# Kernel optimization log

Hardware: AMD Instinct MI355X
Metric: run time of the kernel (lower is better)

## Reference

```python
import jax, jax.numpy as jnp
import numpy as np

N_VISITS, N_PROC, N_MED = 64, 32, 16
V_DIAG, V_PROC, V_MED = 2000, 1500, 4000
EMB, EMB_FF = 256, 128


def _normalize(adj):
    # row-normalize(adj + I), matching GCN.normalize
    adj = adj + np.eye(adj.shape[0], dtype=np.float32)
    rs = adj.sum(1)
    rinv = np.where(rs > 0, 1.0 / rs, 0.0).astype(np.float32)
    return (adj * rinv[:, None]).astype(np.float32)


def setup_inputs() -> dict:
    key = jax.random.key(0)
    ks = jax.random.split(key, 24)
    rng = np.random.default_rng(0)
    ehr = (rng.random((V_MED, V_MED)) < 0.01).astype(np.float32)
    ddi = (rng.random((V_MED, V_MED)) < 0.01).astype(np.float32)
    s = 0.02
    return {
        'proc_codes': jax.random.randint(ks[0], (N_VISITS, N_PROC), 0, V_DIAG + V_PROC + 2),
        'med_codes': jax.random.randint(ks[1], (N_VISITS, N_MED), 0, V_MED),
        'emb_table': jax.random.normal(ks[2], (V_DIAG + V_PROC + 2, EMB_FF)) * s,
        'conv_w': jax.random.normal(ks[3], (3,)) * 0.3,
        'conv_b': jnp.zeros((1,)),
        'wq': jax.random.normal(ks[4], (EMB_FF, EMB)) * s,
        'wk': jax.random.normal(ks[5], (EMB_FF, EMB)) * s,
        'wv': jax.random.normal(ks[6], (EMB_FF, EMB)) * s,
        'wr': jax.random.normal(ks[7], (EMB, EMB)) * s,
        'alpha': jax.random.normal(ks[8], (EMB,)),
        'beta': jax.random.normal(ks[9], (EMB,)),
        'ehr_adj_norm': jnp.asarray(_normalize(ehr)),
        'ddi_adj_norm': jnp.asarray(_normalize(ddi)),
        'ddi_adj_raw': jnp.asarray(ddi),
        'ehr_w1': jax.random.normal(ks[10], (V_MED, EMB)) * s,
        'ehr_b1': jnp.zeros((EMB,)),
        'ehr_w2': jax.random.normal(ks[11], (EMB, EMB)) * s,
        'ehr_b2': jnp.zeros((EMB,)),
        'ddi_w1': jax.random.normal(ks[12], (V_MED, EMB)) * s,
        'ddi_b1': jnp.zeros((EMB,)),
        'ddi_w2': jax.random.normal(ks[13], (EMB, EMB)) * s,
        'ddi_b2': jnp.zeros((EMB,)),
        'inter': jax.random.normal(ks[14], (1,)) * 0.1,
        'out_w1': jax.random.normal(ks[15], (3 * EMB, 2 * EMB)) * s,
        'out_b1': jnp.zeros((2 * EMB,)),
        'out_w2': jax.random.normal(ks[16], (2 * EMB, V_MED)) * s,
        'out_b2': jnp.zeros((V_MED,)),
    }


def _fastformer(x, wq, wk, wv, wr, alpha, beta):
    # x: (1, n, EMB_FF); additive linear attention (all-ones mask => no-op)
    q = x @ wq  # (1, n, EMB)
    k = x @ wk
    v = x @ wv
    scale = EMB ** -0.5
    aw = jax.nn.softmax(q * alpha * scale, axis=-1)
    gq = jnp.sum(q * aw, axis=1)              # global query (1, EMB)
    p = gq[:, None, :] * k                    # (1, n, EMB)
    bw = jax.nn.softmax(p * beta * scale, axis=-1)
    gk = jnp.sum(p * bw, axis=1)              # global key (1, EMB)
    return (gk[:, None, :] * v) @ wr + q


def _gcn(adj, w1, b1, w2, b2):
    # input x = I, so first layer support is just w1
    h = jax.nn.relu(adj @ w1 + b1)
    return adj @ (h @ w2) + b2


def reference(proc_codes, med_codes, emb_table, conv_w, conv_b, wq, wk, wv, wr, alpha, beta,
              ehr_adj_norm, ddi_adj_norm, ddi_adj_raw,
              ehr_w1, ehr_b1, ehr_w2, ehr_b2, ddi_w1, ddi_b1, ddi_w2, ddi_b2,
              inter, out_w1, out_b1, out_w2, out_b2):
    n = proc_codes.shape[0]
    # per-admission mean embedding  (n, EMB_FF)
    i2 = emb_table[proc_codes].mean(axis=1)
    # Conv1d(1,1,k=3,same) over the feature dim, then ReLU
    xp = jnp.pad(i2, ((0, 0), (1, 1)))
    i2 = jax.nn.relu(conv_w[0] * xp[:, :-2] + conv_w[1] * xp[:, 1:-1] + conv_w[2] * xp[:, 2:] + conv_b)
    feat = _fastformer(i2[None], wq, wk, wv, wr, alpha, beta)[0]  # (n, EMB)
    query = feat[-1:]
    drug_memory = _gcn(ehr_adj_norm, ehr_w1, ehr_b1, ehr_w2, ehr_b2) \
        - _gcn(ddi_adj_norm, ddi_w1, ddi_b1, ddi_w2, ddi_b2) * inter[0]
    key_w1 = jax.nn.softmax(query @ drug_memory.T, axis=-1)   # (1, V_MED)
    fact1 = key_w1 @ drug_memory                              # (1, EMB)
    # history (len(input) > 1): multi-hot med history values
    history_keys = feat[:-1]
    hv = jnp.zeros((n - 1, V_MED), dtype=feat.dtype)
    hv = hv.at[jnp.arange(n - 1)[:, None], med_codes[:-1]].set(1.0)
    visit_w = jax.nn.softmax(query @ history_keys.T, axis=-1)
    fact2 = (visit_w @ hv) @ drug_memory
    h = jnp.concatenate([query, fact1, fact2], axis=-1)       # (1, 3*EMB)
    result = jax.nn.relu(h @ out_w1 + out_b1) @ out_w2 + out_b2
    sp = jax.nn.sigmoid(result)[0]
    batch_neg = 0.0005 * jnp.einsum('i,ij,j->', sp, ddi_adj_raw, sp)
    return result, batch_neg
```

## Files before the change

kernel.cpp:

```cpp
#include <hip/hip_runtime.h>
#include <hip/hip_bf16.h>

#define NV 64
#define NP 32
#define NM 16
#define VMED 4000
#define EMB 256
#define EMBFF 128
#define CAP 128
#define GR 4


__device__ __forceinline__ float block_sum_256(float v, float* red) {
    int t = threadIdx.x;
    red[t] = v; __syncthreads();
    for (int s = 128; s > 0; s >>= 1) { if (t < s) red[t] += red[t + s]; __syncthreads(); }
    float r = red[0]; __syncthreads();
    return r;
}
__device__ __forceinline__ float block_max_256(float v, float* red) {
    int t = threadIdx.x;
    red[t] = v; __syncthreads();
    for (int s = 128; s > 0; s >>= 1) { if (t < s) red[t] = fmaxf(red[t], red[t + s]); __syncthreads(); }
    float r = red[0]; __syncthreads();
    return r;
}

__global__ void k_ff1(const int* __restrict__ proc, const float* __restrict__ emb,
                      const float* __restrict__ cw, const float* __restrict__ cb,
                      const float* __restrict__ wq, const float* __restrict__ wk,
                      const float* __restrict__ wv, const float* __restrict__ alpha,
                      float* __restrict__ q, float* __restrict__ k, float* __restrict__ v,
                      float* __restrict__ qaw) {
    __shared__ float sm[EMBFF + 2];
    __shared__ float x[EMBFF];
    __shared__ float red[256];
    int vi = blockIdx.x, t = threadIdx.x;
    if (t < EMBFF) {
        float s = 0.f;
        for (int c = 0; c < NP; c++) s += emb[proc[vi * NP + c] * EMBFF + t];
        sm[t + 1] = s * (1.0f / NP);
    }
    if (t == 0) { sm[0] = 0.f; sm[EMBFF + 1] = 0.f; }
    __syncthreads();
    if (t < EMBFF) {
        float o = cw[0] * sm[t] + cw[1] * sm[t + 1] + cw[2] * sm[t + 2] + cb[0];
        x[t] = o > 0.f ? o : 0.f;
    }
    __syncthreads();
    float aq = 0, ak = 0, av = 0;
    for (int e = 0; e < EMBFF; e++) {
        float xe = x[e];
        aq += xe * wq[e * EMB + t];
        ak += xe * wk[e * EMB + t];
        av += xe * wv[e * EMB + t];
    }
    q[vi * EMB + t] = aq; k[vi * EMB + t] = ak; v[vi * EMB + t] = av;
    const float scale = 0.0625f;
    float z = aq * alpha[t] * scale;
    float m = block_max_256(z, red);
    float e_ = __expf(z - m);
    float sum = block_sum_256(e_, red);
    qaw[vi * EMB + t] = aq * (e_ / sum);
}

__global__ void k_pbw(const float* __restrict__ qaw, const float* __restrict__ k,
                      const float* __restrict__ beta, float* __restrict__ pbw) {
    __shared__ float red[256];
    int vi = blockIdx.x, f = threadIdx.x;
    float g = 0;
    for (int r = 0; r < NV; r++) g += qaw[r * EMB + f];
    float p = g * k[vi * EMB + f];
    const float scale = 0.0625f;
    float z = p * beta[f] * scale;
    float m = block_max_256(z, red);
    float e_ = __expf(z - m);
    float sum = block_sum_256(e_, red);
    pbw[vi * EMB + f] = p * (e_ / sum);
}

__global__ void k_feat(const float* __restrict__ pbw, const float* __restrict__ v,
                       const float* __restrict__ q, const float* __restrict__ wr,
                       float* __restrict__ feat) {
    __shared__ float s[EMB];
    int vi = blockIdx.x, f = threadIdx.x;
    float g = 0;
    for (int r = 0; r < NV; r++) g += pbw[r * EMB + f];
    s[f] = g * v[vi * EMB + f];
    __syncthreads();
    float acc = 0;
    for (int e = 0; e < EMB; e++) acc += s[e] * wr[e * EMB + f];
    feat[vi * EMB + f] = acc + q[vi * EMB + f];
}

__global__ void k_visitw_wmed(const float* __restrict__ feat, const int* __restrict__ med,
                              float* __restrict__ w_med) {
    __shared__ float qs[EMB];
    __shared__ float vw[64];
    __shared__ float red[256];
    __shared__ float wm[VMED];
    int t = threadIdx.x;
    for (int e = t; e < EMB; e += 256) qs[e] = feat[63 * EMB + e];
    for (int i = t; i < VMED; i += 256) wm[i] = 0.f;
    __syncthreads();
    float sc = -1e30f;
    if (t < 63) {
        float a = 0;
        for (int e = 0; e < EMB; e++) a += qs[e] * feat[t * EMB + e];
        sc = a;
    }
    float m = block_max_256(sc, red);
    float e_ = (t < 63) ? __expf(sc - m) : 0.f;
    float sum = block_sum_256(e_, red);
    if (t < 63) vw[t] = e_ / sum;
    __syncthreads();
    for (int i = t; i < 63 * NM; i += 256) {
        int vv = i / NM, mm = i % NM;
        int code = med[vv * NM + mm];
        bool dup = false;
        for (int m2 = 0; m2 < mm; m2++)
            if (med[vv * NM + m2] == code) dup = true;
        if (!dup) atomicAdd(&wm[code], vw[vv]);
    }
    __syncthreads();
    for (int i = t; i < VMED; i += 256) w_med[i] = wm[i];
}

__global__ void k_gcn(const float* __restrict__ eadj, const float* __restrict__ dadj,
                      const float* __restrict__ ew1, const float* __restrict__ eb1,
                      const float* __restrict__ ew2,
                      const float* __restrict__ dw1, const float* __restrict__ db1,
                      const float* __restrict__ dw2,
                      float* __restrict__ outE, float* __restrict__ outD,
                      int* __restrict__ ccntE, int* __restrict__ cidxE, float* __restrict__ cvalE,
                      int* __restrict__ ccntD, int* __restrict__ cidxD, float* __restrict__ cvalD) {
    __shared__ float x[GR][EMB];
    __shared__ int idx[GR][CAP];
    __shared__ float val[GR][CAP];
    __shared__ int cnt[GR];
    int b = blockIdx.x, t = threadIdx.x;
    bool isD = b >= 1000;
    const float* adj = isD ? dadj : eadj;
    const float* w1  = isD ? dw1  : ew1;
    const float* b1  = isD ? db1  : eb1;
    const float* w2  = isD ? dw2  : ew2;
    float* outp = isD ? outD : outE;
    int*   ccnt = isD ? ccntD : ccntE;
    int*   cidx = isD ? cidxD : cidxE;
    float* cval = isD ? cvalD : cvalE;
    int r0 = (isD ? b - 1000 : b) * GR;
    if (t < GR) cnt[t] = 0;
    __syncthreads();

    const float4* base4 = (const float4*)(adj + (size_t)r0 * VMED);
    const int Q = VMED / 4;
    for (int jj = t; jj < GR * Q; jj += 256) {
        float4 a = base4[jj];
        int r = jj / Q;
        int c0 = (jj - r * Q) * 4;
        if (a.x != 0.f) { int p = atomicAdd(&cnt[r], 1); if (p < CAP) { idx[r][p] = c0;     val[r][p] = a.x; } }
        if (a.y != 0.f) { int p = atomicAdd(&cnt[r], 1); if (p < CAP) { idx[r][p] = c0 + 1; val[r][p] = a.y; } }
        if (a.z != 0.f) { int p = atomicAdd(&cnt[r], 1); if (p < CAP) { idx[r][p] = c0 + 2; val[r][p] = a.z; } }
        if (a.w != 0.f) { int p = atomicAdd(&cnt[r], 1); if (p < CAP) { idx[r][p] = c0 + 3; val[r][p] = a.w; } }
    }
    __syncthreads();

    for (int r = 0; r < GR; r++) {
        int n = cnt[r] < CAP ? cnt[r] : CAP;
        if (t == 0) ccnt[r0 + r] = n;
        if (t < n) { cidx[(r0 + r) * CAP + t] = idx[r][t]; cval[(r0 + r) * CAP + t] = val[r][t]; }
        float acc = b1[t];
        for (int e = 0; e < n; e++) acc += val[r][e] * w1[(size_t)idx[r][e] * EMB + t];
        x[r][t] = acc > 0.f ? acc : 0.f;
    }
    __syncthreads();

    float a[GR];
    #pragma unroll
    for (int r = 0; r < GR; r++) a[r] = 0.f;
    #pragma unroll 4
    for (int e = 0; e < EMB; e++) {
        float we = w2[e * EMB + t];
        #pragma unroll
        for (int r = 0; r < GR; r++) a[r] += x[r][e] * we;
    }
    for (int r = 0; r < GR; r++) outp[(size_t)(r0 + r) * EMB + t] = a[r];
}

__global__ void k_acc(const int* __restrict__ ccntE, const int* __restrict__ cidxE,
                      const float* __restrict__ cvalE,
                      const int* __restrict__ ccntD, const int* __restrict__ cidxD,
                      const float* __restrict__ cvalD,
                      const float* __restrict__ xe, const float* __restrict__ xd,
                      const float* __restrict__ b2e, const float* __restrict__ b2d,
                      const float* __restrict__ inter, const float* __restrict__ feat,
                      float* __restrict__ dm, float* __restrict__ sdm) {
    __shared__ int idxE[CAP];
    __shared__ float valE[CAP];
    __shared__ int idxD[CAP];
    __shared__ float valD[CAP];
    __shared__ float red[256];
    int i = blockIdx.x, t = threadIdx.x;
    int nE = ccntE[i], nD = ccntD[i];
    if (t < nE) { idxE[t] = cidxE[i * CAP + t]; valE[t] = cvalE[i * CAP + t]; }
    if (t < nD) { idxD[t] = cidxD[i * CAP + t]; valD[t] = cvalD[i * CAP + t]; }
    __syncthreads();
    float aE = b2e[t];
    for (int e = 0; e < nE; e++) aE += valE[e] * xe[(size_t)idxE[e] * EMB + t];
    float aD = b2d[t];
    for (int e = 0; e < nD; e++) aD += valD[e] * xd[(size_t)idxD[e] * EMB + t];
    float dmv = aE - inter[0] * aD;
    dm[(size_t)i * EMB + t] = dmv;
    float s = block_sum_256(dmv * feat[63 * EMB + t], red);
    if (t == 0) sdm[i] = s;
}

__global__ void k_softmax4000(const float* __restrict__ s, float* __restrict__ out) {
    __shared__ float red[256];
    int t = threadIdx.x;
    float m = -1e30f;
    for (int i = t; i < VMED; i += 256) m = fmaxf(m, s[i]);
    m = block_max_256(m, red);
    float sum = 0;
    for (int i = t; i < VMED; i += 256) { float e = __expf(s[i] - m); out[i] = e; sum += e; }
    sum = block_sum_256(sum, red);
    float inv = 1.f / sum;
    for (int i = t; i < VMED; i += 256) out[i] *= inv;
}

__global__ void k_facts_part(const float* __restrict__ dm, const float* __restrict__ kw,
                             const float* __restrict__ wm, float* __restrict__ part1,
                             float* __restrict__ part2) {
    int f = threadIdx.x, b = blockIdx.x;
    int r0 = b * 100;
    float a1 = 0, a2 = 0;
    for (int r = r0; r < r0 + 100; r++) {
        float d = dm[(size_t)r * EMB + f];
        a1 += kw[r] * d;
        a2 += wm[r] * d;
    }
    part1[b * EMB + f] = a1;
    part2[b * EMB + f] = a2;
}

__global__ void k_hidden_part(const float* __restrict__ feat, const float* __restrict__ part1,
                              const float* __restrict__ part2, const float* __restrict__ w1,
                              float* __restrict__ hpart) {
    __shared__ float xs[16];
    int b = blockIdx.x, t = threadIdx.x;
    int e0 = b * 16;
    if (t < 16) {
        int e = e0 + t;
        float xv;
        if (e < 256) xv = feat[63 * EMB + e];
        else if (e < 512) { float s = 0; for (int p = 0; p < 40; p++) s += part1[p * EMB + (e - 256)]; xv = s; }
        else              { float s = 0; for (int p = 0; p < 40; p++) s += part2[p * EMB + (e - 512)]; xv = s; }
        xs[t] = xv;
    }
    __syncthreads();
    float a1 = 0, a2 = 0;
    #pragma unroll
    for (int i = 0; i < 16; i++) {
        int e = e0 + i;
        a1 += xs[i] * w1[e * 512 + t];
        a2 += xs[i] * w1[e * 512 + t + 256];
    }
    hpart[b * 512 + t] = a1;
    hpart[b * 512 + t + 256] = a2;
}

__global__ void k_result(const float* __restrict__ hpart, const float* __restrict__ b1,
                         const float* __restrict__ w2, const float* __restrict__ b2,
                         float* __restrict__ out, float* __restrict__ sp) {
    __shared__ float hx[512];
    __shared__ float red[8][32];
    int t = threadIdx.x;
    for (int jj = t; jj < 512; jj += 256) {
        float s = b1[jj];
        for (int p = 0; p < 48; p++) s += hpart[p * 512 + jj];
        hx[jj] = s > 0.f ? s : 0.f;
    }
    __syncthreads();
    int lane = t & 31, seg = t >> 5;
    int j = blockIdx.x * 32 + lane;
    float acc = 0;
    int e0 = seg * 64;
    #pragma unroll 8
    for (int e = e0; e < e0 + 64; e++) acc += hx[e] * w2[(size_t)e * VMED + j];
    red[seg][lane] = acc;
    __syncthreads();
    if (seg == 0) {
        float s = b2[j];
        for (int p = 0; p < 8; p++) s += red[p][lane];
        out[j] = s;
        sp[j] = 1.f / (1.f + __expf(-s));
    }
}

__global__ void k_bneg(const float* __restrict__ ddi, const float* __restrict__ sp,
                       float* __restrict__ bpart) {
    __shared__ float4 spl[VMED / 4];
    __shared__ float red[8][256];
    int t = threadIdx.x;
    const float4* sp4 = (const float4*)sp;
    for (int j4 = t; j4 < VMED / 4; j4 += 256) spl[j4] = sp4[j4];
    __syncthreads();
    int i0 = blockIdx.x * 8;
    const float4* row4 = (const float4*)(ddi + (size_t)i0 * VMED);
    float p[8] = {0, 0, 0, 0, 0, 0, 0, 0};
    for (int j4 = t; j4 < VMED / 4; j4 += 256) {
        float4 s4 = spl[j4];
        #pragma unroll
        for (int rr = 0; rr < 8; rr++) {
            float4 a = row4[rr * (VMED / 4) + j4];
            p[rr] += a.x * s4.x + a.y * s4.y + a.z * s4.z + a.w * s4.w;
        }
    }
    #pragma unroll
    for (int rr = 0; rr < 8; rr++) red[rr][t] = p[rr];
    __syncthreads();
    for (int s = 128; s > 0; s >>= 1) {
        if (t < s) {
            #pragma unroll
            for (int rr = 0; rr < 8; rr++) red[rr][t] += red[rr][t + s];
        }
        __syncthreads();
    }
    if (t < 8) bpart[i0 + t] = sp[i0 + t] * red[t][0];
}

__global__ void FastRx_wo_Diag_19473381720179_kernel(const float* __restrict__ bpart,
                                                     float* __restrict__ out) {
    __shared__ float red[256];
    int t = threadIdx.x;
    float s = 0;
    for (int i = t; i < VMED; i += 256) s += bpart[i];
    s = block_sum_256(s, red);
    if (t == 0) out[VMED] = 0.0005f * s;
}

extern "C" __attribute__((visibility("default")))
void kernel_launch(void* const* d_in, const int* in_sizes, int n_in,
                   void* d_out, int out_size, void* d_ws, size_t ws_size,
                   hipStream_t stream) {
    const int*   proc_codes = (const int*)d_in[0];
    const int*   med_codes  = (const int*)d_in[1];
    const float* emb_table  = (const float*)d_in[2];
    const float* conv_w     = (const float*)d_in[3];
    const float* conv_b     = (const float*)d_in[4];
    const float* wq         = (const float*)d_in[5];
    const float* wk         = (const float*)d_in[6];
    const float* wv         = (const float*)d_in[7];
    const float* wr         = (const float*)d_in[8];
    const float* alpha      = (const float*)d_in[9];
    const float* beta       = (const float*)d_in[10];
    const float* ehr_adj    = (const float*)d_in[11];
    const float* ddi_adj    = (const float*)d_in[12];
    const float* ddi_raw    = (const float*)d_in[13];
    const float* ehr_w1     = (const float*)d_in[14];
    const float* ehr_b1     = (const float*)d_in[15];
    const float* ehr_w2     = (const float*)d_in[16];
    const float* ehr_b2     = (const float*)d_in[17];
    const float* ddi_w1     = (const float*)d_in[18];
    const float* ddi_b1     = (const float*)d_in[19];
    const float* ddi_w2     = (const float*)d_in[20];
    const float* ddi_b2     = (const float*)d_in[21];
    const float* inter      = (const float*)d_in[22];
    const float* out_w1     = (const float*)d_in[23];
    const float* out_b1     = (const float*)d_in[24];
    const float* out_w2     = (const float*)d_in[25];
    const float* out_b2     = (const float*)d_in[26];
    float* out = (float*)d_out;

    float* w = (float*)d_ws;
    float* q      = w;
    float* k      = w + 16384;
    float* v      = w + 32768;
    float* tmpA   = w + 49152;
    float* tmpB   = w + 65536;
    float* feat   = w + 81920;
    float* wmed   = w + 98304;
    float* sdm    = w + 102400;
    float* sp     = w + 106496;
    float* bufA   = w + 110592;
    float* bufC   = bufA + 1024000;
    float* bufB   = bufC + 1024000;
    int*   ccntE  = (int*)(bufB + 1024000);
    int*   cidxE  = ccntE + 4096;
    float* cvalE  = (float*)(cidxE + 512000);
    int*   ccntD  = (int*)(cvalE + 512000);
    int*   cidxD  = ccntD + 4096;
    float* cvalD  = (float*)(cidxD + 512000);
    float* part1  = bufA;
    float* part2  = bufA + 10240;
    float* hpart  = bufA + 20480;
    float* bpart  = bufA + 45056;

    k_ff1<<<NV, EMB, 0, stream>>>(proc_codes, emb_table, conv_w, conv_b,
                                  wq, wk, wv, alpha, q, k, v, tmpA);
    k_pbw<<<NV, EMB, 0, stream>>>(tmpA, k, beta, tmpB);
    k_feat<<<NV, EMB, 0, stream>>>(tmpB, v, q, wr, feat);
    k_visitw_wmed<<<1, 256, 0, stream>>>(feat, med_codes, wmed);

    k_gcn<<<2000, 256, 0, stream>>>(ehr_adj, ddi_adj,
                                    ehr_w1, ehr_b1, ehr_w2,
                                    ddi_w1, ddi_b1, ddi_w2,
                                    bufA, bufC,
                                    ccntE, cidxE, cvalE, ccntD, cidxD, cvalD);
    k_acc<<<VMED, 256, 0, stream>>>(ccntE, cidxE, cvalE, ccntD, cidxD, cvalD,
                                    bufA, bufC, ehr_b2, ddi_b2, inter, feat,
                                    bufB, sdm);

    k_softmax4000<<<1, 256, 0, stream>>>(sdm, sdm);
    k_facts_part<<<40, 256, 0, stream>>>(bufB, sdm, wmed, part1, part2);
    k_hidden_part<<<48, 256, 0, stream>>>(feat, part1, part2, out_w1, hpart);
    k_result<<<125, 256, 0, stream>>>(hpart, out_b1, out_w2, out_b2, out, sp);
    k_bneg<<<VMED / 8, 256, 0, stream>>>(ddi_raw, sp, bpart);
    FastRx_wo_Diag_19473381720179_kernel<<<1, 256, 0, stream>>>(bpart, out);
}
```

Before: 409.1 us.

## Split GCN into per-row sparse scan kernel and batched gather-matmul kernel

After: 412.9 us. About the same (+0.9%).

```diff
diff --git a/kernel.cpp b/kernel.cpp
--- a/kernel.cpp
+++ b/kernel.cpp
@@ -8,7 +8,6 @@
 #define EMB 256
 #define EMBFF 128
 #define CAP 128
-#define GR 4
 
 
 __device__ __forceinline__ float block_sum_256(float v, float* red) {
@@ -126,65 +125,95 @@
     for (int i = t; i < VMED; i += 256) w_med[i] = wm[i];
 }
 
-__global__ void k_gcn(const float* __restrict__ eadj, const float* __restrict__ dadj,
-                      const float* __restrict__ ew1, const float* __restrict__ eb1,
-                      const float* __restrict__ ew2,
-                      const float* __restrict__ dw1, const float* __restrict__ db1,
-                      const float* __restrict__ dw2,
-                      float* __restrict__ outE, float* __restrict__ outD,
-                      int* __restrict__ ccntE, int* __restrict__ cidxE, float* __restrict__ cvalE,
-                      int* __restrict__ ccntD, int* __restrict__ cidxD, float* __restrict__ cvalD) {
-    __shared__ float x[GR][EMB];
-    __shared__ int idx[GR][CAP];
-    __shared__ float val[GR][CAP];
-    __shared__ int cnt[GR];
+__global__ void k_scan(const float* __restrict__ eadj, const float* __restrict__ dadj,
+                       int* __restrict__ ccntE, int* __restrict__ cidxE, float* __restrict__ cvalE,
+                       int* __restrict__ ccntD, int* __restrict__ cidxD, float* __restrict__ cvalD) {
+    __shared__ int idx[CAP];
+    __shared__ float val[CAP];
+    __shared__ int cnt;
     int b = blockIdx.x, t = threadIdx.x;
-    bool isD = b >= 1000;
+    bool isD = b >= VMED;
+    int i = isD ? b - VMED : b;
     const float* adj = isD ? dadj : eadj;
-    const float* w1  = isD ? dw1  : ew1;
-    const float* b1  = isD ? db1  : eb1;
-    const float* w2  = isD ? dw2  : ew2;
-    float* outp = isD ? outD : outE;
     int*   ccnt = isD ? ccntD : ccntE;
     int*   cidx = isD ? cidxD : cidxE;
     float* cval = isD ? cvalD : cvalE;
-    int r0 = (isD ? b - 1000 : b) * GR;
-    if (t < GR) cnt[t] = 0;
-    __syncthreads();
-
-    const float4* base4 = (const float4*)(adj + (size_t)r0 * VMED);
-    const int Q = VMED / 4;
-    for (int jj = t; jj < GR * Q; jj += 256) {
-        float4 a = base4[jj];
-        int r = jj / Q;
-        int c0 = (jj - r * Q) * 4;
-        if (a.x != 0.f) { int p = atomicAdd(&cnt[r], 1); if (p < CAP) { idx[r][p] = c0;     val[r][p] = a.x; } }
-        if (a.y != 0.f) { int p = atomicAdd(&cnt[r], 1); if (p < CAP) { idx[r][p] = c0 + 1; val[r][p] = a.y; } }
-        if (a.z != 0.f) { int p = atomicAdd(&cnt[r], 1); if (p < CAP) { idx[r][p] = c0 + 2; val[r][p] = a.z; } }
-        if (a.w != 0.f) { int p = atomicAdd(&cnt[r], 1); if (p < CAP) { idx[r][p] = c0 + 3; val[r][p] = a.w; } }
-    }
-    __syncthreads();
-
-    for (int r = 0; r < GR; r++) {
-        int n = cnt[r] < CAP ? cnt[r] : CAP;
-        if (t == 0) ccnt[r0 + r] = n;
-        if (t < n) { cidx[(r0 + r) * CAP + t] = idx[r][t]; cval[(r0 + r) * CAP + t] = val[r][t]; }
+    if (t == 0) cnt = 0;
+    __syncthreads();
+    const float4* row4 = (const float4*)(adj + (size_t)i * VMED);
+    for (int j4 = t; j4 < VMED / 4; j4 += 256) {
+        float4 a = row4[j4];
+        int c0 = j4 * 4;
+        if (a.x != 0.f) { int p = atomicAdd(&cnt, 1); if (p < CAP) { idx[p] = c0;     val[p] = a.x; } }
+        if (a.y != 0.f) { int p = atomicAdd(&cnt, 1); if (p < CAP) { idx[p] = c0 + 1; val[p] = a.y; } }
+        if (a.z != 0.f) { int p = atomicAdd(&cnt, 1); if (p < CAP) { idx[p] = c0 + 2; val[p] = a.z; } }
+        if (a.w != 0.f) { int p = atomicAdd(&cnt, 1); if (p < CAP) { idx[p] = c0 + 3; val[p] = a.w; } }
+    }
+    __syncthreads();
+    int n = cnt < CAP ? cnt : CAP;
+    if (t == 0) ccnt[i] = n;
+    if (t < n) { cidx[i * CAP + t] = idx[t]; cval[i * CAP + t] = val[t]; }
+}
+
+__global__ void k_gcn2(const int* __restrict__ ccntE, const int* __restrict__ cidxE,
+                       const float* __restrict__ cvalE,
+                       const int* __restrict__ ccntD, const int* __restrict__ cidxD,
+                       const float* __restrict__ cvalD,
+                       const float* __restrict__ ew1, const float* __restrict__ eb1,
+                       const float* __restrict__ ew2,
+                       const float* __restrict__ dw1, const float* __restrict__ db1,
+                       const float* __restrict__ dw2,
+                       float* __restrict__ outE, float* __restrict__ outD) {
+    __shared__ float x[8][EMB];
+    __shared__ int idx[8][CAP];
+    __shared__ float val[8][CAP];
+    __shared__ int nn8[8];
+    int b = blockIdx.x, t = threadIdx.x;
+    bool isD = b >= 500;
+    const int*   ccnt = isD ? ccntD : ccntE;
+    const int*   cidx = isD ? cidxD : cidxE;
+    const float* cval = isD ? cvalD : cvalE;
+    const float* w1   = isD ? dw1 : ew1;
+    const float* b1   = isD ? db1 : eb1;
+    const float* w2   = isD ? dw2 : ew2;
+    float* outp = isD ? outD : outE;
+    int r0 = (isD ? b - 500 : b) * 8;
+    for (int r = 0; r < 8; r++) {
+        int n = ccnt[r0 + r];
+        int n8 = (n + 7) & ~7;
+        if (t == 0) nn8[r] = n8;
+        if (t < n) { idx[r][t] = cidx[(r0 + r) * CAP + t]; val[r][t] = cval[(r0 + r) * CAP + t]; }
+        else if (t < n8) { idx[r][t] = 0; val[r][t] = 0.f; }
+    }
+    __syncthreads();
+    for (int r = 0; r < 8; r++) {
         float acc = b1[t];
-        for (int e = 0; e < n; e++) acc += val[r][e] * w1[(size_t)idx[r][e] * EMB + t];
+        int n8 = nn8[r];
+        for (int e = 0; e < n8; e += 8) {
+            float g0 = w1[(size_t)idx[r][e]     * EMB + t];
+            float g1 = w1[(size_t)idx[r][e + 1] * EMB + t];
+            float g2 = w1[(size_t)idx[r][e + 2] * EMB + t];
+            float g3 = w1[(size_t)idx[r][e + 3] * EMB + t];
+            float g4 = w1[(size_t)idx[r][e + 4] * EMB + t];
+            float g5 = w1[(size_t)idx[r][e + 5] * EMB + t];
+            float g6 = w1[(size_t)idx[r][e + 6] * EMB + t];
+            float g7 = w1[(size_t)idx[r][e + 7] * EMB + t];
+            acc += val[r][e]     * g0 + val[r][e + 1] * g1
+                 + val[r][e + 2] * g2 + val[r][e + 3] * g3
+                 + val[r][e + 4] * g4 + val[r][e + 5] * g5
+                 + val[r][e + 6] * g6 + val[r][e + 7] * g7;
+        }
         x[r][t] = acc > 0.f ? acc : 0.f;
     }
     __syncthreads();
-
-    float a[GR];
-    #pragma unroll
-    for (int r = 0; r < GR; r++) a[r] = 0.f;
+    float a[8] = {0, 0, 0, 0, 0, 0, 0, 0};
     #pragma unroll 4
     for (int e = 0; e < EMB; e++) {
         float we = w2[e * EMB + t];
         #pragma unroll
-        for (int r = 0; r < GR; r++) a[r] += x[r][e] * we;
-    }
-    for (int r = 0; r < GR; r++) outp[(size_t)(r0 + r) * EMB + t] = a[r];
+        for (int r = 0; r < 8; r++) a[r] += x[r][e] * we;
+    }
+    for (int r = 0; r < 8; r++) outp[(size_t)(r0 + r) * EMB + t] = a[r];
 }
 
 __global__ void k_acc(const int* __restrict__ ccntE, const int* __restrict__ cidxE,
@@ -202,13 +231,38 @@
     __shared__ float red[256];
     int i = blockIdx.x, t = threadIdx.x;
     int nE = ccntE[i], nD = ccntD[i];
+    int nE8 = (nE + 7) & ~7, nD8 = (nD + 7) & ~7;
     if (t < nE) { idxE[t] = cidxE[i * CAP + t]; valE[t] = cvalE[i * CAP + t]; }
+    else if (t < nE8) { idxE[t] = 0; valE[t] = 0.f; }
     if (t < nD) { idxD[t] = cidxD[i * CAP + t]; valD[t] = cvalD[i * CAP + t]; }
+    else if (t < nD8) { idxD[t] = 0; valD[t] = 0.f; }
     __syncthreads();
     float aE = b2e[t];
-    for (int e = 0; e < nE; e++) aE += valE[e] * xe[(size_t)idxE[e] * EMB + t];
+    for (int e = 0; e < nE8; e += 8) {
+        float g0 = xe[(size_t)idxE[e]     * EMB + t];
+        float g1 = xe[(size_t)idxE[e + 1] * EMB + t];
+        float g2 = xe[(size_t)idxE[e + 2] * EMB + t];
+        float g3 = xe[(size_t)idxE[e + 3] * EMB + t];
+        float g4 = xe[(size_t)idxE[e + 4] * EMB + t];
+        float g5 = xe[(size_t)idxE[e + 5] * EMB + t];
+        float g6 = xe[(size_t)idxE[e + 6] * EMB + t];
+        float g7 = xe[(size_t)idxE[e + 7] * EMB + t];
+        aE += valE[e] * g0 + valE[e + 1] * g1 + valE[e + 2] * g2 + valE[e + 3] * g3
+            + valE[e + 4] * g4 + valE[e + 5] * g5 + valE[e + 6] * g6 + valE[e + 7] * g7;
+    }
     float aD = b2d[t];
-    for (int e = 0; e < nD; e++) aD += valD[e] * xd[(size_t)idxD[e] * EMB + t];
+    for (int e = 0; e < nD8; e += 8) {
+        float g0 = xd[(size_t)idxD[e]     * EMB + t];
+        float g1 = xd[(size_t)idxD[e + 1] * EMB + t];
+        float g2 = xd[(size_t)idxD[e + 2] * EMB + t];
+        float g3 = xd[(size_t)idxD[e + 3] * EMB + t];
+        float g4 = xd[(size_t)idxD[e + 4] * EMB + t];
+        float g5 = xd[(size_t)idxD[e + 5] * EMB + t];
+        float g6 = xd[(size_t)idxD[e + 6] * EMB + t];
+        float g7 = xd[(size_t)idxD[e + 7] * EMB + t];
+        aD += valD[e] * g0 + valD[e + 1] * g1 + valD[e + 2] * g2 + valD[e + 3] * g3
+            + valD[e + 4] * g4 + valD[e + 5] * g5 + valD[e + 6] * g6 + valD[e + 7] * g7;
+    }
     float dmv = aE - inter[0] * aD;
     dm[(size_t)i * EMB + t] = dmv;
     float s = block_sum_256(dmv * feat[63 * EMB + t], red);
@@ -402,11 +456,12 @@
     k_feat<<<NV, EMB, 0, stream>>>(tmpB, v, q, wr, feat);
     k_visitw_wmed<<<1, 256, 0, stream>>>(feat, med_codes, wmed);
 
-    k_gcn<<<2000, 256, 0, stream>>>(ehr_adj, ddi_adj,
-                                    ehr_w1, ehr_b1, ehr_w2,
-                                    ddi_w1, ddi_b1, ddi_w2,
-                                    bufA, bufC,
-                                    ccntE, cidxE, cvalE, ccntD, cidxD, cvalD);
+    k_scan<<<2 * VMED, 256, 0, stream>>>(ehr_adj, ddi_adj,
+                                         ccntE, cidxE, cvalE, ccntD, cidxD, cvalD);
+    k_gcn2<<<1000, 256, 0, stream>>>(ccntE, cidxE, cvalE, ccntD, cidxD, cvalD,
+                                     ehr_w1, ehr_b1, ehr_w2,
+                                     ddi_w1, ddi_b1, ddi_w2,
+                                     bufA, bufC);
     k_acc<<<VMED, 256, 0, stream>>>(ccntE, cidxE, cvalE, ccntD, cidxD, cvalD,
                                     bufA, bufC, ehr_b2, ddi_b2, inter, feat,
                                     bufB, sdm);
```
